# Kernel tuning notes

Measured on AMD Instinct MI355X. Metric: run time of the kernel, lower is better.

## Reference

```python
import jax, jax.numpy as jnp
import numpy as np

N_ATOM_FEATS = 64
N_RBF = 10
N_CONV = 3
N_HIDDEN = 64
N_NODES = 50000
N_EDGES = 800000
N_GRAPHS = 512


def setup_inputs() -> dict:
    key = jax.random.key(0)
    ks = jax.random.split(key, 32)
    d = {}
    d["x_ids"] = jax.random.randint(ks[0], (N_NODES,), 0, 95)
    d["edge_index"] = jax.random.randint(ks[1], (2, N_EDGES), 0, N_NODES)
    d["edge_attr"] = jax.random.uniform(ks[2], (N_EDGES,), jnp.float32) * 6.0  # distances in [0,6)
    d["batch"] = jnp.sort(jax.random.randint(ks[3], (N_NODES,), 0, N_GRAPHS))
    # parameters
    def lin(k, fan_in, shape):
        return jax.random.normal(k, shape, jnp.float32) / np.sqrt(fan_in)
    d["emb"] = jax.random.normal(ks[4], (95, N_ATOM_FEATS), jnp.float32)
    d["blk_W1"] = lin(ks[5], N_ATOM_FEATS, (N_CONV, N_ATOM_FEATS, N_ATOM_FEATS))
    d["blk_b1"] = jnp.zeros((N_CONV, N_ATOM_FEATS), jnp.float32)
    d["blk_We"] = lin(ks[6], N_RBF, (N_CONV, N_RBF, N_ATOM_FEATS))
    d["blk_be"] = jnp.zeros((N_CONV, N_ATOM_FEATS), jnp.float32)
    d["blk_W2"] = lin(ks[7], N_ATOM_FEATS, (N_CONV, N_ATOM_FEATS, N_ATOM_FEATS))
    d["blk_b2"] = jnp.zeros((N_CONV, N_ATOM_FEATS), jnp.float32)
    d["Ws"] = lin(ks[8], N_ATOM_FEATS, (N_ATOM_FEATS, 2 * N_HIDDEN))
    d["bs"] = jnp.zeros((2 * N_HIDDEN,), jnp.float32)
    d["Wbg1"] = lin(ks[9], 2 * N_HIDDEN, (2 * N_HIDDEN, N_HIDDEN))
    d["bbg1"] = jnp.zeros((N_HIDDEN,), jnp.float32)
    d["Wbg2"] = lin(ks[10], N_HIDDEN, (N_HIDDEN, 1))
    d["bbg2"] = jnp.zeros((1,), jnp.float32)
    d["Weh1"] = lin(ks[11], 2 * N_HIDDEN, (2 * N_HIDDEN, N_HIDDEN))
    d["beh1"] = jnp.zeros((N_HIDDEN,), jnp.float32)
    d["Weh2"] = lin(ks[12], N_HIDDEN, (N_HIDDEN, 1))
    d["beh2"] = jnp.zeros((1,), jnp.float32)
    return d


def reference(x_ids, edge_index, edge_attr, batch, emb,
              blk_W1, blk_b1, blk_We, blk_be, blk_W2, blk_b2,
              Ws, bs, Wbg1, bbg1, Wbg2, bbg2, Weh1, beh1, Weh2, beh2):
    src, dst = edge_index[0], edge_index[1]
    # embedding lookup [N, F]
    x = emb[x_ids]
    # Gaussian smearing RBF: [E, n_rbf]
    offset = jnp.linspace(0.0, 6.0, N_RBF).astype(edge_attr.dtype)
    coeff = -0.5 / (offset[1] - offset[0]) ** 2
    e = jnp.exp(coeff * (edge_attr[:, None] - offset) ** 2)
    # interaction blocks (SchNet-style CFConv with residual)
    for i in range(N_CONV):
        h = x @ blk_W1[i] + blk_b1[i]                     # [N, F]
        f = e @ blk_We[i] + blk_be[i]                     # [E, F] edge filters
        m = h[src] * f                                    # [E, F] messages
        agg = jax.ops.segment_sum(m, dst, num_segments=N_NODES)
        x = x + agg @ blk_W2[i] + blk_b2[i]
        x = jax.nn.softplus(x)
    # global mean pool over graphs
    sums = jax.ops.segment_sum(x, batch, num_segments=N_GRAPHS)
    cnts = jax.ops.segment_sum(jnp.ones((x.shape[0],), x.dtype), batch, num_segments=N_GRAPHS)
    c = sums / jnp.maximum(cnts, 1.0)[:, None]
    c = jax.nn.relu(c @ Ws + bs)                          # [G, 2H]
    out_bg = jax.nn.relu(c @ Wbg1 + bbg1) @ Wbg2 + bbg2   # [G, 1]
    out_eh = jax.nn.relu(c @ Weh1 + beh1) @ Weh2 + beh2   # [G, 1]
    return (out_bg, out_eh)
```

## Files before the change

### kernel.cpp

```cpp
#include <hip/hip_runtime.h>
#include <hip/hip_fp16.h>
#include <cstddef>


#define RBF_C0 1.0f
#define RBF_C1 0.60653065971f
#define RBF_C2 0.13533528324f
#define RBF_C3 0.011108996538f
#define RBF_C4 3.3546262790e-4f
#define RBF_C5 3.7266531720e-6f
#define RBF_C6 1.5229979745e-8f
#define RBF_C7 2.2897348457e-11f
#define RBF_C8 1.2664165549e-14f
#define RBF_C9 2.5767043600e-18f

__device__ __forceinline__ float softplusf(float v) {
    return fmaxf(v, 0.0f) + log1pf(__expf(-fabsf(v)));
}

__device__ __forceinline__ float row_gemv(const float4* __restrict__ xr,
                                          const float w[64], float bj) {
    float a0 = bj, a1 = 0.f, a2 = 0.f, a3 = 0.f;
#pragma unroll
    for (int q = 0; q < 4; ++q) {
        float4 v0 = xr[4 * q + 0], v1 = xr[4 * q + 1];
        float4 v2 = xr[4 * q + 2], v3 = xr[4 * q + 3];
        a0 = fmaf(v0.x, w[16 * q + 0], a0);  a0 = fmaf(v0.y, w[16 * q + 1], a0);
        a0 = fmaf(v0.z, w[16 * q + 2], a0);  a0 = fmaf(v0.w, w[16 * q + 3], a0);
        a1 = fmaf(v1.x, w[16 * q + 4], a1);  a1 = fmaf(v1.y, w[16 * q + 5], a1);
        a1 = fmaf(v1.z, w[16 * q + 6], a1);  a1 = fmaf(v1.w, w[16 * q + 7], a1);
        a2 = fmaf(v2.x, w[16 * q + 8], a2);  a2 = fmaf(v2.y, w[16 * q + 9], a2);
        a2 = fmaf(v2.z, w[16 * q + 10], a2); a2 = fmaf(v2.w, w[16 * q + 11], a2);
        a3 = fmaf(v3.x, w[16 * q + 12], a3); a3 = fmaf(v3.y, w[16 * q + 13], a3);
        a3 = fmaf(v3.z, w[16 * q + 14], a3); a3 = fmaf(v3.w, w[16 * q + 15], a3);
    }
    return (a0 + a1) + (a2 + a3);
}

__device__ __forceinline__ float filt_ab(const float wp[10], float bj, float A, float B) {
    float P = wp[9];
    P = fmaf(B, P, wp[8]); P = fmaf(B, P, wp[7]); P = fmaf(B, P, wp[6]);
    P = fmaf(B, P, wp[5]); P = fmaf(B, P, wp[4]); P = fmaf(B, P, wp[3]);
    P = fmaf(B, P, wp[2]); P = fmaf(B, P, wp[1]); P = fmaf(B, P, wp[0]);
    return fmaf(A, P, bj);
}

__global__ void k_pre(const int* __restrict__ dst, int* __restrict__ deg,
                      const int* __restrict__ batch, int* __restrict__ gstart,
                      const int* __restrict__ ids, const float* __restrict__ emb,
                      const float* __restrict__ W1, const float* __restrict__ b1,
                      float* __restrict__ x, __half* __restrict__ hA,
                      int n_edges, int n_nodes, int n_graphs) {
    int tid = blockIdx.x * blockDim.x + threadIdx.x;
    int nth = gridDim.x * blockDim.x;
    for (int e = tid; e < n_edges; e += nth) atomicAdd(&deg[dst[e]], 1);
    for (int n = tid; n < n_nodes; n += nth) {
        int b = batch[n];
        int prev = (n == 0) ? -1 : batch[n - 1];
        for (int g = prev + 1; g <= b; ++g) gstart[g] = n;
        if (n == n_nodes - 1)
            for (int g = b + 1; g <= n_graphs; ++g) gstart[g] = n_nodes;
    }
    int lane = threadIdx.x & 63;
    int gw = __builtin_amdgcn_readfirstlane(tid >> 6);
    int nw = nth >> 6;
    float w[64];
#pragma unroll
    for (int k = 0; k < 64; ++k) w[k] = W1[k * 64 + lane];
    float bj = b1[lane];
    for (int n = gw; n < n_nodes; n += nw) {
        int id = __builtin_amdgcn_readfirstlane(ids[n]);
        const float4* xr = (const float4*)(emb + id * 64);
        float v = row_gemv(xr, w, bj);
        x[n * 64 + lane] = emb[id * 64 + lane];
        hA[n * 64 + lane] = __float2half(v);
    }
}

__global__ void k_scana(const int* __restrict__ deg, int* __restrict__ off_,
                        int* __restrict__ bsum, int n) {
    __shared__ int s[256];
    int i = blockIdx.x * 256 + threadIdx.x;
    int v = (i < n) ? deg[i] : 0;
    s[threadIdx.x] = v;
    __syncthreads();
    for (int off = 1; off < 256; off <<= 1) {
        int t = (threadIdx.x >= off) ? s[threadIdx.x - off] : 0;
        __syncthreads();
        s[threadIdx.x] += t;
        __syncthreads();
    }
    if (i < n) off_[i + 1] = s[threadIdx.x];
    if (threadIdx.x == 255) bsum[blockIdx.x] = s[255];
}

__global__ void k_scanb(int* __restrict__ bsum, int nb) {
    __shared__ int s[256];
    int v = ((int)threadIdx.x < nb) ? bsum[threadIdx.x] : 0;
    s[threadIdx.x] = v;
    __syncthreads();
    for (int off = 1; off < 256; off <<= 1) {
        int t = (threadIdx.x >= off) ? s[threadIdx.x - off] : 0;
        __syncthreads();
        s[threadIdx.x] += t;
        __syncthreads();
    }
    if ((int)threadIdx.x < nb) bsum[threadIdx.x] = s[threadIdx.x] - v;
}

__global__ void k_scanc(const int* __restrict__ deg, const int* __restrict__ bsum,
                        int* __restrict__ off_, int* __restrict__ cursor, int n) {
    int i = blockIdx.x * blockDim.x + threadIdx.x;
    if (i < n) {
        int incl = off_[i + 1] + bsum[i >> 8];
        off_[i + 1] = incl;
        cursor[i] = incl - deg[i];
    }
    if (i == 0) off_[0] = 0;
}

__global__ void k_scatter(const int* __restrict__ src, const int* __restrict__ dst,
                          const float* __restrict__ dist, int* __restrict__ cursor,
                          int4* __restrict__ psort, int n_edges) {
    int e = blockIdx.x * blockDim.x + threadIdx.x;
    if (e >= n_edges) return;
    int t = dst[e];
    int pos = atomicAdd(&cursor[t], 1);
    float d = dist[e];
    float A = __expf(-1.125f * d * d);
    float B = __expf(1.5f * d);
    psort[pos] = make_int4(src[e] << 6, __float_as_int(A), __float_as_int(B), 0);
}

__global__ __launch_bounds__(256, 8) void k_gather(
        const int4* __restrict__ ps, const int* __restrict__ off,
        const __half* __restrict__ h,
        const float* __restrict__ We, const float* __restrict__ be,
        float* __restrict__ agg, int n_nodes) {
    int lane = threadIdx.x & 63;
    int gw = __builtin_amdgcn_readfirstlane((blockIdx.x * blockDim.x + threadIdx.x) >> 6);
    int nw = (gridDim.x * blockDim.x) >> 6;

    const float C[10] = {RBF_C0, RBF_C1, RBF_C2, RBF_C3, RBF_C4,
                         RBF_C5, RBF_C6, RBF_C7, RBF_C8, RBF_C9};
    float wp[10];
#pragma unroll
    for (int r = 0; r < 10; ++r) wp[r] = We[r * 64 + lane] * C[r];
    float bj = be[lane];

    for (int n = gw; n < n_nodes; n += nw) {
        int k0 = off[n], k1 = off[n + 1];
        float acc = 0.0f;
        int k = k0;
        for (; k + 8 <= k1; k += 8) {
            int4 p0 = ps[k + 0], p1 = ps[k + 1], p2 = ps[k + 2], p3 = ps[k + 3];
            int4 p4 = ps[k + 4], p5 = ps[k + 5], p6 = ps[k + 6], p7 = ps[k + 7];
            float g0 = __half2float(h[p0.x + lane]);
            float g1 = __half2float(h[p1.x + lane]);
            float g2 = __half2float(h[p2.x + lane]);
            float g3 = __half2float(h[p3.x + lane]);
            float g4 = __half2float(h[p4.x + lane]);
            float g5 = __half2float(h[p5.x + lane]);
            float g6 = __half2float(h[p6.x + lane]);
            float g7 = __half2float(h[p7.x + lane]);
            acc = fmaf(g0, filt_ab(wp, bj, __int_as_float(p0.y), __int_as_float(p0.z)), acc);
            acc = fmaf(g1, filt_ab(wp, bj, __int_as_float(p1.y), __int_as_float(p1.z)), acc);
            acc = fmaf(g2, filt_ab(wp, bj, __int_as_float(p2.y), __int_as_float(p2.z)), acc);
            acc = fmaf(g3, filt_ab(wp, bj, __int_as_float(p3.y), __int_as_float(p3.z)), acc);
            acc = fmaf(g4, filt_ab(wp, bj, __int_as_float(p4.y), __int_as_float(p4.z)), acc);
            acc = fmaf(g5, filt_ab(wp, bj, __int_as_float(p5.y), __int_as_float(p5.z)), acc);
            acc = fmaf(g6, filt_ab(wp, bj, __int_as_float(p6.y), __int_as_float(p6.z)), acc);
            acc = fmaf(g7, filt_ab(wp, bj, __int_as_float(p7.y), __int_as_float(p7.z)), acc);
        }
        for (; k + 4 <= k1; k += 4) {
            int4 p0 = ps[k + 0], p1 = ps[k + 1], p2 = ps[k + 2], p3 = ps[k + 3];
            float g0 = __half2float(h[p0.x + lane]);
            float g1 = __half2float(h[p1.x + lane]);
            float g2 = __half2float(h[p2.x + lane]);
            float g3 = __half2float(h[p3.x + lane]);
            acc = fmaf(g0, filt_ab(wp, bj, __int_as_float(p0.y), __int_as_float(p0.z)), acc);
            acc = fmaf(g1, filt_ab(wp, bj, __int_as_float(p1.y), __int_as_float(p1.z)), acc);
            acc = fmaf(g2, filt_ab(wp, bj, __int_as_float(p2.y), __int_as_float(p2.z)), acc);
            acc = fmaf(g3, filt_ab(wp, bj, __int_as_float(p3.y), __int_as_float(p3.z)), acc);
        }
        for (; k < k1; ++k) {
            int4 p = ps[k];
            float g = __half2float(h[p.x + lane]);
            acc = fmaf(g, filt_ab(wp, bj, __int_as_float(p.y), __int_as_float(p.z)), acc);
        }
        agg[n * 64 + lane] = acc;
    }
}

__global__ __launch_bounds__(256) void k_epi(
        const float* __restrict__ agg, float* __restrict__ x,
        const float* __restrict__ W2, const float* __restrict__ b2,
        const float* __restrict__ W1n, const float* __restrict__ b1n,
        __half* __restrict__ hout, int n_nodes, int do_next) {
    __shared__ float B1[64 * 65];
    const int t = threadIdx.x;
    const int lane = t & 63;
    const int wid = __builtin_amdgcn_readfirstlane(t >> 6);
    const int base = blockIdx.x << 6;
    const int nv = min(64, n_nodes - base);

#pragma unroll
    for (int i = 0; i < 4; ++i) {
        int f = ((wid * 4 + i) << 8) + (lane << 2);
        int r = f >> 6, c = f & 63;
        int rs = min(r, nv - 1);
        const float4 v = *(const float4*)(agg + (((size_t)(base + rs)) << 6) + c);
        B1[r * 65 + c + 0] = v.x; B1[r * 65 + c + 1] = v.y;
        B1[r * 65 + c + 2] = v.z; B1[r * 65 + c + 3] = v.w;
    }
    __syncthreads();

    float o[16];
#pragma unroll
    for (int jj = 0; jj < 16; ++jj) o[jj] = 0.0f;
#pragma unroll 4
    for (int k = 0; k < 64; ++k) {
        float a = B1[lane * 65 + k];
        const float* w = W2 + (k << 6) + (wid << 4);
#pragma unroll
        for (int jj = 0; jj < 16; ++jj) o[jj] = fmaf(a, w[jj], o[jj]);
    }
    __syncthreads();

#pragma unroll
    for (int i = 0; i < 4; ++i) {
        int f = ((wid * 4 + i) << 8) + (lane << 2);
        int r = f >> 6, c = f & 63;
        int rs = min(r, nv - 1);
        const float4 v = *(const float4*)(x + (((size_t)(base + rs)) << 6) + c);
        B1[r * 65 + c + 0] = v.x; B1[r * 65 + c + 1] = v.y;
        B1[r * 65 + c + 2] = v.z; B1[r * 65 + c + 3] = v.w;
    }
    __syncthreads();

#pragma unroll
    for (int jj = 0; jj < 16; ++jj) {
        int j = (wid << 4) + jj;
        float xv = B1[lane * 65 + j];
        float xn = softplusf(xv + o[jj] + b2[j]);
        B1[lane * 65 + j] = xn;
    }
    __syncthreads();

#pragma unroll
    for (int rr = 0; rr < 16; ++rr) {
        int r = (wid << 4) + rr;
        if (r < nv) x[(((size_t)(base + r)) << 6) + lane] = B1[r * 65 + lane];
    }

    if (do_next) {
        float o2[16];
#pragma unroll
        for (int jj = 0; jj < 16; ++jj) o2[jj] = b1n[(wid << 4) + jj];
#pragma unroll 4
        for (int k = 0; k < 64; ++k) {
            float xk = B1[lane * 65 + k];
            const float* w = W1n + (k << 6) + (wid << 4);
#pragma unroll
            for (int jj = 0; jj < 16; ++jj) o2[jj] = fmaf(xk, w[jj], o2[jj]);
        }
        __syncthreads();
#pragma unroll
        for (int jj = 0; jj < 16; ++jj)
            B1[lane * 65 + (wid << 4) + jj] = o2[jj];
        __syncthreads();
#pragma unroll
        for (int rr = 0; rr < 16; ++rr) {
            int r = (wid << 4) + rr;
            if (r < nv)
                hout[(((size_t)(base + r)) << 6) + lane] = __float2half(B1[r * 65 + lane]);
        }
    }
}

__global__ __launch_bounds__(256, 6) void k_conv(
        const int4* __restrict__ ps, const int* __restrict__ off,
        const __half* __restrict__ h,
        const float* __restrict__ We, const float* __restrict__ be,
        const float* __restrict__ W2, const float* __restrict__ b2,
        const float* __restrict__ W1n, const float* __restrict__ b1n,
        float* __restrict__ x, __half* __restrict__ hout,
        int n_nodes, int do_next) {
    int lane = threadIdx.x & 63;
    int gw = __builtin_amdgcn_readfirstlane((blockIdx.x * blockDim.x + threadIdx.x) >> 6);
    int nw = (gridDim.x * blockDim.x) >> 6;

    const float C[10] = {RBF_C0, RBF_C1, RBF_C2, RBF_C3, RBF_C4,
                         RBF_C5, RBF_C6, RBF_C7, RBF_C8, RBF_C9};
    float wp[10];
#pragma unroll
    for (int r = 0; r < 10; ++r) wp[r] = We[r * 64 + lane] * C[r];
    float bj  = be[lane];
    float b2j = b2[lane];
    float b1j = do_next ? b1n[lane] : 0.0f;

    for (int n = gw; n < n_nodes; n += nw) {
        int k0 = off[n], k1 = off[n + 1];
        float acc = 0.0f;
        int k = k0;
        for (; k + 8 <= k1; k += 8) {
            int4 p0 = ps[k + 0], p1 = ps[k + 1], p2 = ps[k + 2], p3 = ps[k + 3];
            int4 p4 = ps[k + 4], p5 = ps[k + 5], p6 = ps[k + 6], p7 = ps[k + 7];
            float g0 = __half2float(h[p0.x + lane]);
            float g1 = __half2float(h[p1.x + lane]);
            float g2 = __half2float(h[p2.x + lane]);
            float g3 = __half2float(h[p3.x + lane]);
            float g4 = __half2float(h[p4.x + lane]);
            float g5 = __half2float(h[p5.x + lane]);
            float g6 = __half2float(h[p6.x + lane]);
            float g7 = __half2float(h[p7.x + lane]);
            acc = fmaf(g0, filt_ab(wp, bj, __int_as_float(p0.y), __int_as_float(p0.z)), acc);
            acc = fmaf(g1, filt_ab(wp, bj, __int_as_float(p1.y), __int_as_float(p1.z)), acc);
            acc = fmaf(g2, filt_ab(wp, bj, __int_as_float(p2.y), __int_as_float(p2.z)), acc);
            acc = fmaf(g3, filt_ab(wp, bj, __int_as_float(p3.y), __int_as_float(p3.z)), acc);
            acc = fmaf(g4, filt_ab(wp, bj, __int_as_float(p4.y), __int_as_float(p4.z)), acc);
            acc = fmaf(g5, filt_ab(wp, bj, __int_as_float(p5.y), __int_as_float(p5.z)), acc);
            acc = fmaf(g6, filt_ab(wp, bj, __int_as_float(p6.y), __int_as_float(p6.z)), acc);
            acc = fmaf(g7, filt_ab(wp, bj, __int_as_float(p7.y), __int_as_float(p7.z)), acc);
        }
        for (; k + 4 <= k1; k += 4) {
            int4 p0 = ps[k + 0], p1 = ps[k + 1], p2 = ps[k + 2], p3 = ps[k + 3];
            float g0 = __half2float(h[p0.x + lane]);
            float g1 = __half2float(h[p1.x + lane]);
            float g2 = __half2float(h[p2.x + lane]);
            float g3 = __half2float(h[p3.x + lane]);
            acc = fmaf(g0, filt_ab(wp, bj, __int_as_float(p0.y), __int_as_float(p0.z)), acc);
            acc = fmaf(g1, filt_ab(wp, bj, __int_as_float(p1.y), __int_as_float(p1.z)), acc);
            acc = fmaf(g2, filt_ab(wp, bj, __int_as_float(p2.y), __int_as_float(p2.z)), acc);
            acc = fmaf(g3, filt_ab(wp, bj, __int_as_float(p3.y), __int_as_float(p3.z)), acc);
        }
        for (; k < k1; ++k) {
            int4 p = ps[k];
            float g = __half2float(h[p.x + lane]);
            acc = fmaf(g, filt_ab(wp, bj, __int_as_float(p.y), __int_as_float(p.z)), acc);
        }
        float o0 = b2j + x[n * 64 + lane];
        float o1 = 0.f, o2 = 0.f, o3 = 0.f;
#pragma unroll 4
        for (int kk = 0; kk < 16; ++kk) {
            o0 = fmaf(__shfl(acc, kk),      W2[(kk)      * 64 + lane], o0);
            o1 = fmaf(__shfl(acc, kk + 16), W2[(kk + 16) * 64 + lane], o1);
            o2 = fmaf(__shfl(acc, kk + 32), W2[(kk + 32) * 64 + lane], o2);
            o3 = fmaf(__shfl(acc, kk + 48), W2[(kk + 48) * 64 + lane], o3);
        }
        float xn = softplusf((o0 + o1) + (o2 + o3));
        x[n * 64 + lane] = xn;
        if (do_next) {
            float q0 = b1j, q1 = 0.f, q2 = 0.f, q3 = 0.f;
#pragma unroll 4
            for (int kk = 0; kk < 16; ++kk) {
                q0 = fmaf(__shfl(xn, kk),      W1n[(kk)      * 64 + lane], q0);
                q1 = fmaf(__shfl(xn, kk + 16), W1n[(kk + 16) * 64 + lane], q1);
                q2 = fmaf(__shfl(xn, kk + 32), W1n[(kk + 32) * 64 + lane], q2);
                q3 = fmaf(__shfl(xn, kk + 48), W1n[(kk + 48) * 64 + lane], q3);
            }
            hout[n * 64 + lane] = __float2half((q0 + q1) + (q2 + q3));
        }
    }
}

__global__ void k_poolhead(const float* __restrict__ x, const int* __restrict__ gstart,
                           const float* __restrict__ Ws, const float* __restrict__ bs,
                           const float* __restrict__ Wbg1, const float* __restrict__ bbg1,
                           const float* __restrict__ Wbg2, const float* __restrict__ bbg2,
                           const float* __restrict__ Weh1, const float* __restrict__ beh1,
                           const float* __restrict__ Weh2, const float* __restrict__ beh2,
                           float* __restrict__ out, int n_graphs) {
    __shared__ float red[256];
    __shared__ float c[64];
    __shared__ float h1[128];
    int g = blockIdx.x;
    int t = threadIdx.x, j = t & 63, part = t >> 6;
    int s0 = gstart[g], s1 = gstart[g + 1];
    float acc = 0.0f;
    for (int n = s0 + part; n < s1; n += 4) acc += x[n * 64 + j];
    red[t] = acc;
    __syncthreads();
    if (part == 0)
        c[j] = (red[j] + red[64 + j] + red[128 + j] + red[192 + j]) /
               fmaxf((float)(s1 - s0), 1.0f);
    __syncthreads();
    if (t < 128) {
        float av = bs[t];
#pragma unroll 8
        for (int k = 0; k < 64; ++k) av = fmaf(c[k], Ws[k * 128 + t], av);
        h1[t] = fmaxf(av, 0.0f);
    }
    __syncthreads();
    if (t < 128) {
        const float* W1p = (t < 64) ? Wbg1 : Weh1;
        const float* b1p = (t < 64) ? bbg1 : beh1;
        const float* W2p = (t < 64) ? Wbg2 : Weh2;
        float b2v = (t < 64) ? bbg2[0] : beh2[0];
        int ln = t & 63;
        float a2 = b1p[ln];
#pragma unroll 8
        for (int k = 0; k < 128; ++k) a2 = fmaf(h1[k], W1p[k * 64 + ln], a2);
        a2 = fmaxf(a2, 0.0f);
        float pr = a2 * W2p[ln];
#pragma unroll
        for (int off = 32; off > 0; off >>= 1) pr += __shfl_down(pr, off);
        if (ln == 0) out[(t < 64 ? 0 : n_graphs) + g] = pr + b2v;
    }
}

extern "C" void kernel_launch(void* const* d_in, const int* in_sizes, int n_in,
                              void* d_out, int out_size, void* d_ws, size_t ws_size,
                              hipStream_t stream) {
    const int*   x_ids = (const int*)d_in[0];
    const int*   eidx  = (const int*)d_in[1];
    const float* eattr = (const float*)d_in[2];
    const int*   batch = (const int*)d_in[3];
    const float* emb   = (const float*)d_in[4];
    const float* W1    = (const float*)d_in[5];
    const float* b1    = (const float*)d_in[6];
    const float* We    = (const float*)d_in[7];
    const float* be    = (const float*)d_in[8];
    const float* W2    = (const float*)d_in[9];
    const float* b2    = (const float*)d_in[10];
    const float* Ws_   = (const float*)d_in[11];
    const float* bs_   = (const float*)d_in[12];
    const float* Wbg1  = (const float*)d_in[13];
    const float* bbg1  = (const float*)d_in[14];
    const float* Wbg2  = (const float*)d_in[15];
    const float* bbg2  = (const float*)d_in[16];
    const float* Weh1  = (const float*)d_in[17];
    const float* beh1  = (const float*)d_in[18];
    const float* Weh2  = (const float*)d_in[19];
    const float* beh2  = (const float*)d_in[20];

    int n_nodes  = in_sizes[0];
    int n_edges  = in_sizes[2];
    int n_graphs = out_size / 2;
    const int* src = eidx;
    const int* dst = eidx + n_edges;

    size_t base_bytes =
        (size_t)n_nodes * 64 * sizeof(float)
      + (size_t)n_nodes * 64 * sizeof(__half) * 2
      + (size_t)n_edges * sizeof(int4)
      + (size_t)n_nodes * sizeof(int) * 2
      + (size_t)(n_nodes + 1) * sizeof(int)
      + 256 * sizeof(int)
      + (size_t)(n_graphs + 1) * sizeof(int);
    size_t agg_bytes = (size_t)n_nodes * 64 * sizeof(float);
    int use_split = (ws_size >= base_bytes + agg_bytes + 1024) ? 1 : 0;

    char* p = (char*)d_ws;
    float* x     = (float*)p;   p += (size_t)n_nodes * 64 * sizeof(float);
    __half* hA   = (__half*)p;  p += (size_t)n_nodes * 64 * sizeof(__half);
    __half* hB   = (__half*)p;  p += (size_t)n_nodes * 64 * sizeof(__half);
    int4* psort  = (int4*)p;    p += (size_t)n_edges * sizeof(int4);
    int* deg     = (int*)p;     p += (size_t)n_nodes * sizeof(int);
    int* off_    = (int*)p;     p += (size_t)(n_nodes + 1) * sizeof(int);
    int* cursor  = (int*)p;     p += (size_t)n_nodes * sizeof(int);
    int* bsum    = (int*)p;     p += 256 * sizeof(int);
    int* gstart  = (int*)p;     p += (size_t)(n_graphs + 1) * sizeof(int);
    float* agg   = (float*)p;   p += agg_bytes;
    float* out   = (float*)d_out;

    int nchunks = (n_nodes + 255) / 256;
    int nbE = (n_edges + 255) / 256;
    int nbN = (n_nodes + 255) / 256;
    int ntile = (n_nodes + 63) / 64;

    hipMemsetAsync(deg, 0, (size_t)n_nodes * sizeof(int), stream);
    k_pre<<<nbE, 256, 0, stream>>>(dst, deg, batch, gstart, x_ids, emb, W1, b1,
                                   x, hA, n_edges, n_nodes, n_graphs);
    k_scana<<<nchunks, 256, 0, stream>>>(deg, off_, bsum, n_nodes);
    k_scanb<<<1, 256, 0, stream>>>(bsum, nchunks);
    k_scanc<<<nbN, 256, 0, stream>>>(deg, bsum, off_, cursor, n_nodes);
    k_scatter<<<nbE, 256, 0, stream>>>(src, dst, eattr, cursor, psort, n_edges);

    if (use_split) {
        k_gather<<<4096, 256, 0, stream>>>(psort, off_, hA, We, be, agg, n_nodes);
        k_epi<<<ntile, 256, 0, stream>>>(agg, x, W2, b2,
                                         W1 + 4096, b1 + 64, hB, n_nodes, 1);
        k_gather<<<4096, 256, 0, stream>>>(psort, off_, hB, We + 640, be + 64, agg, n_nodes);
        k_epi<<<ntile, 256, 0, stream>>>(agg, x, W2 + 4096, b2 + 64,
                                         W1 + 8192, b1 + 128, hA, n_nodes, 1);
        k_gather<<<4096, 256, 0, stream>>>(psort, off_, hA, We + 1280, be + 128, agg, n_nodes);
        k_epi<<<ntile, 256, 0, stream>>>(agg, x, W2 + 8192, b2 + 128,
                                         nullptr, nullptr, nullptr, n_nodes, 0);
    } else {
        k_conv<<<4096, 256, 0, stream>>>(psort, off_, hA, We, be, W2, b2,
                                         W1 + 4096, b1 + 64, x, hB, n_nodes, 1);
        k_conv<<<4096, 256, 0, stream>>>(psort, off_, hB, We + 640, be + 64,
                                         W2 + 4096, b2 + 64,
                                         W1 + 8192, b1 + 128, x, hA, n_nodes, 1);
        k_conv<<<4096, 256, 0, stream>>>(psort, off_, hA, We + 1280, be + 128,
                                         W2 + 8192, b2 + 128,
                                         nullptr, nullptr, x, nullptr, n_nodes, 0);
    }

    k_poolhead<<<n_graphs, 256, 0, stream>>>(x, gstart, Ws_, bs_, Wbg1, bbg1, Wbg2, bbg2,
                                             Weh1, beh1, Weh2, beh2, out, n_graphs);
}
```

Measured before the change: 385.1 us.

## Split CSR edge scatter into two-pass bucketed scatter for write locality

Replaces the single random-position edge scatter with a two-pass scheme. The first pass scatters edges into coarse buckets of 32 destination nodes. The second pass reads those bucketed edges and scatters them to their final CSR positions, so writes land in a much narrower address range and cache locality improves. This adds an extra read and write of an 800k-entry int4 buffer plus a second kernel launch. The temporary buffer reuses the agg workspace region.

```diff
diff --git a/kernel.cpp b/kernel.cpp
--- a/kernel.cpp
+++ b/kernel.cpp
@@ -2,6 +2,8 @@
 #include <hip/hip_fp16.h>
 #include <cstddef>
 
+
+#define BSHIFT 5
 
 #define RBF_C0 1.0f
 #define RBF_C1 0.60653065971f
@@ -109,14 +111,40 @@
 }
 
 __global__ void k_scanc(const int* __restrict__ deg, const int* __restrict__ bsum,
-                        int* __restrict__ off_, int* __restrict__ cursor, int n) {
+                        int* __restrict__ off_, int* __restrict__ cursor,
+                        int* __restrict__ bcursor, int n) {
     int i = blockIdx.x * blockDim.x + threadIdx.x;
     if (i < n) {
         int incl = off_[i + 1] + bsum[i >> 8];
         off_[i + 1] = incl;
         cursor[i] = incl - deg[i];
-    }
-    if (i == 0) off_[0] = 0;
+        if (((i + 1) & ((1 << BSHIFT) - 1)) == 0)
+            bcursor[(i + 1) >> BSHIFT] = incl;
+    }
+    if (i == 0) { off_[0] = 0; bcursor[0] = 0; }
+}
+
+__global__ void k_scat1(const int* __restrict__ src, const int* __restrict__ dst,
+                        const float* __restrict__ dist, int* __restrict__ bcursor,
+                        int4* __restrict__ tmp, int n_edges) {
+    int e = blockIdx.x * blockDim.x + threadIdx.x;
+    if (e >= n_edges) return;
+    int t = dst[e];
+    int pos = atomicAdd(&bcursor[t >> BSHIFT], 1);
+    float d = dist[e];
+    float A = __expf(-1.125f * d * d);
+    float B = __expf(1.5f * d);
+    tmp[pos] = make_int4(src[e] << 6, __float_as_int(A), __float_as_int(B), t);
+}
+
+__global__ void k_scat2(const int4* __restrict__ tmp, int* __restrict__ cursor,
+                        int4* __restrict__ psort, int n_edges) {
+    int e = blockIdx.x * blockDim.x + threadIdx.x;
+    if (e >= n_edges) return;
+    int4 p = tmp[e];
+    int t = p.w;
+    int pos = atomicAdd(&cursor[t], 1);
+    psort[pos] = p;
 }
 
 __global__ void k_scatter(const int* __restrict__ src, const int* __restrict__ dst,
@@ -439,6 +467,7 @@
     int n_graphs = out_size / 2;
     const int* src = eidx;
     const int* dst = eidx + n_edges;
+    int nbuck = ((n_nodes + (1 << BSHIFT) - 1) >> BSHIFT);
 
     size_t base_bytes =
         (size_t)n_nodes * 64 * sizeof(float)
@@ -447,9 +476,12 @@
       + (size_t)n_nodes * sizeof(int) * 2
       + (size_t)(n_nodes + 1) * sizeof(int)
       + 256 * sizeof(int)
-      + (size_t)(n_graphs + 1) * sizeof(int);
+      + (size_t)(n_graphs + 1) * sizeof(int)
+      + (size_t)(nbuck + 1) * sizeof(int);
     size_t agg_bytes = (size_t)n_nodes * 64 * sizeof(float);
-    int use_split = (ws_size >= base_bytes + agg_bytes + 1024) ? 1 : 0;
+    size_t tmp_bytes = (size_t)n_edges * sizeof(int4);
+    size_t aggtmp_bytes = agg_bytes > tmp_bytes ? agg_bytes : tmp_bytes;
+    int use_split = (ws_size >= base_bytes + aggtmp_bytes + 1024) ? 1 : 0;
 
     char* p = (char*)d_ws;
     float* x     = (float*)p;   p += (size_t)n_nodes * 64 * sizeof(float);
@@ -461,7 +493,9 @@
     int* cursor  = (int*)p;     p += (size_t)n_nodes * sizeof(int);
     int* bsum    = (int*)p;     p += 256 * sizeof(int);
     int* gstart  = (int*)p;     p += (size_t)(n_graphs + 1) * sizeof(int);
-    float* agg   = (float*)p;   p += agg_bytes;
+    int* bcursor = (int*)p;     p += (size_t)(nbuck + 1) * sizeof(int);
+    float* agg   = (float*)p;
+    int4* tmp    = (int4*)p;
     float* out   = (float*)d_out;
 
     int nchunks = (n_nodes + 255) / 256;
@@ -474,10 +508,11 @@
                                    x, hA, n_edges, n_nodes, n_graphs);
     k_scana<<<nchunks, 256, 0, stream>>>(deg, off_, bsum, n_nodes);
     k_scanb<<<1, 256, 0, stream>>>(bsum, nchunks);
-    k_scanc<<<nbN, 256, 0, stream>>>(deg, bsum, off_, cursor, n_nodes);
-    k_scatter<<<nbE, 256, 0, stream>>>(src, dst, eattr, cursor, psort, n_edges);
+    k_scanc<<<nbN, 256, 0, stream>>>(deg, bsum, off_, cursor, bcursor, n_nodes);
 
     if (use_split) {
+        k_scat1<<<nbE, 256, 0, stream>>>(src, dst, eattr, bcursor, tmp, n_edges);
+        k_scat2<<<nbE, 256, 0, stream>>>(tmp, cursor, psort, n_edges);
         k_gather<<<4096, 256, 0, stream>>>(psort, off_, hA, We, be, agg, n_nodes);
         k_epi<<<ntile, 256, 0, stream>>>(agg, x, W2, b2,
                                          W1 + 4096, b1 + 64, hB, n_nodes, 1);
@@ -488,6 +523,7 @@
         k_epi<<<ntile, 256, 0, stream>>>(agg, x, W2 + 8192, b2 + 128,
                                          nullptr, nullptr, nullptr, n_nodes, 0);
     } else {
+        k_scatter<<<nbE, 256, 0, stream>>>(src, dst, eattr, cursor, psort, n_edges);
         k_conv<<<4096, 256, 0, stream>>>(psort, off_, hA, We, be, W2, b2,
                                          W1 + 4096, b1 + 64, x, hB, n_nodes, 1);
         k_conv<<<4096, 256, 0, stream>>>(psort, off_, hB, We + 640, be + 64,
```

New measurement: 491.4 us. 1.28x slower.

## Replace random atomic edge scatter with two-pass bucketed counting sort

Applied to the files above, without the earlier changes.

Edge sorting by destination now runs in two passes instead of one. First, each block bins 1024 edges into 256-node buckets in shared memory and writes them contiguously into a temporary buffer at per-bucket cursors. Second, one block per bucket places edges into their final CSR slots. The aim is to replace scattered 16-byte global writes and contended global atomics with locality-friendly writes. In exchange it adds an extra full pass over the edge payload, reuses the aggregation buffer as scratch, and only handles up to 256 buckets in the shared histogram.

```diff
diff --git a/kernel.cpp b/kernel.cpp
--- a/kernel.cpp
+++ b/kernel.cpp
@@ -2,6 +2,8 @@
 #include <hip/hip_fp16.h>
 #include <cstddef>
 
+
+#define BSH 8
 
 #define RBF_C0 1.0f
 #define RBF_C1 0.60653065971f
@@ -109,14 +111,96 @@
 }
 
 __global__ void k_scanc(const int* __restrict__ deg, const int* __restrict__ bsum,
-                        int* __restrict__ off_, int* __restrict__ cursor, int n) {
+                        int* __restrict__ off_, int* __restrict__ cursor,
+                        int* __restrict__ bcursor, int n) {
     int i = blockIdx.x * blockDim.x + threadIdx.x;
     if (i < n) {
         int incl = off_[i + 1] + bsum[i >> 8];
         off_[i + 1] = incl;
         cursor[i] = incl - deg[i];
-    }
-    if (i == 0) off_[0] = 0;
+        if (((i + 1) & ((1 << BSH) - 1)) == 0)
+            bcursor[(i + 1) >> BSH] = incl;
+    }
+    if (i == 0) { off_[0] = 0; bcursor[0] = 0; }
+}
+
+__global__ __launch_bounds__(256) void k_scat1(
+        const int* __restrict__ src, const int* __restrict__ dst,
+        const float* __restrict__ dist, int* __restrict__ bcursor,
+        int4* __restrict__ tmp, int n_edges) {
+    __shared__ int hist[256], sofs[256], hbase[256], lcur[256];
+    __shared__ int4 buf[1024];
+    const int t = threadIdx.x;
+    const int base = blockIdx.x << 10;
+
+    hist[t] = 0;
+    __syncthreads();
+
+    int bk[4]; int4 pl[4];
+#pragma unroll
+    for (int i = 0; i < 4; ++i) {
+        int e = base + (i << 8) + t;
+        if (e < n_edges) {
+            int d_ = dst[e];
+            float dd = dist[e];
+            float A = __expf(-1.125f * dd * dd);
+            float B = __expf(1.5f * dd);
+            pl[i] = make_int4(src[e] << 6, __float_as_int(A), __float_as_int(B), d_);
+            bk[i] = d_ >> BSH;
+            atomicAdd(&hist[bk[i]], 1);
+        } else bk[i] = -1;
+    }
+    __syncthreads();
+
+    int mycnt = hist[t];
+    for (int off = 1; off < 256; off <<= 1) {
+        int v = (t >= off) ? hist[t - off] : 0;
+        __syncthreads();
+        hist[t] += v;
+        __syncthreads();
+    }
+    sofs[t] = hist[t] - mycnt;
+    lcur[t] = hist[t] - mycnt;
+    if (mycnt > 0) hbase[t] = atomicAdd(&bcursor[t], mycnt);
+    __syncthreads();
+
+#pragma unroll
+    for (int i = 0; i < 4; ++i) {
+        if (bk[i] >= 0) {
+            int ls = atomicAdd(&lcur[bk[i]], 1);
+            buf[ls] = pl[i];
+        }
+    }
+    __syncthreads();
+
+    int tot = n_edges - base; if (tot > 1024) tot = 1024;
+    for (int s = t; s < tot; s += 256) {
+        int4 p = buf[s];
+        int b = p.w >> BSH;
+        tmp[hbase[b] + (s - sofs[b])] = p;
+    }
+}
+
+__global__ __launch_bounds__(256) void k_scat2(
+        const int4* __restrict__ tmp, const int* __restrict__ off_,
+        int* __restrict__ cursor, int4* __restrict__ psort, int n_nodes) {
+    int b = blockIdx.x;
+    int s0 = off_[b << BSH];
+    int hi = (b + 1) << BSH; if (hi > n_nodes) hi = n_nodes;
+    int s1 = off_[hi];
+    int s = s0 + threadIdx.x;
+    for (; s + 768 < s1; s += 1024) {
+        int4 p0 = tmp[s], p1 = tmp[s + 256], p2 = tmp[s + 512], p3 = tmp[s + 768];
+        int q0 = atomicAdd(&cursor[p0.w], 1);
+        int q1 = atomicAdd(&cursor[p1.w], 1);
+        int q2 = atomicAdd(&cursor[p2.w], 1);
+        int q3 = atomicAdd(&cursor[p3.w], 1);
+        psort[q0] = p0; psort[q1] = p1; psort[q2] = p2; psort[q3] = p3;
+    }
+    for (; s < s1; s += 256) {
+        int4 p = tmp[s];
+        psort[atomicAdd(&cursor[p.w], 1)] = p;
+    }
 }
 
 __global__ void k_scatter(const int* __restrict__ src, const int* __restrict__ dst,
@@ -439,6 +523,8 @@
     int n_graphs = out_size / 2;
     const int* src = eidx;
     const int* dst = eidx + n_edges;
+    int nbuck = (n_nodes + (1 << BSH) - 1) >> BSH;
+    int nbc = (nbuck < 256 ? 256 : nbuck) + 4;
 
     size_t base_bytes =
         (size_t)n_nodes * 64 * sizeof(float)
@@ -447,9 +533,12 @@
       + (size_t)n_nodes * sizeof(int) * 2
       + (size_t)(n_nodes + 1) * sizeof(int)
       + 256 * sizeof(int)
-      + (size_t)(n_graphs + 1) * sizeof(int);
+      + (size_t)(n_graphs + 1) * sizeof(int)
+      + (size_t)nbc * sizeof(int);
     size_t agg_bytes = (size_t)n_nodes * 64 * sizeof(float);
-    int use_split = (ws_size >= base_bytes + agg_bytes + 1024) ? 1 : 0;
+    size_t tmp_bytes = (size_t)n_edges * sizeof(int4);
+    size_t aggtmp_bytes = agg_bytes > tmp_bytes ? agg_bytes : tmp_bytes;
+    int use_split = (ws_size >= base_bytes + aggtmp_bytes + 1024) ? 1 : 0;
 
     char* p = (char*)d_ws;
     float* x     = (float*)p;   p += (size_t)n_nodes * 64 * sizeof(float);
@@ -461,23 +550,27 @@
     int* cursor  = (int*)p;     p += (size_t)n_nodes * sizeof(int);
     int* bsum    = (int*)p;     p += 256 * sizeof(int);
     int* gstart  = (int*)p;     p += (size_t)(n_graphs + 1) * sizeof(int);
-    float* agg   = (float*)p;   p += agg_bytes;
+    int* bcursor = (int*)p;     p += (size_t)nbc * sizeof(int);
+    float* agg   = (float*)p;
+    int4* tmp    = (int4*)p;
     float* out   = (float*)d_out;
 
     int nchunks = (n_nodes + 255) / 256;
     int nbE = (n_edges + 255) / 256;
     int nbN = (n_nodes + 255) / 256;
     int ntile = (n_nodes + 63) / 64;
+    int nbS1 = (n_edges + 1023) / 1024;
 
     hipMemsetAsync(deg, 0, (size_t)n_nodes * sizeof(int), stream);
     k_pre<<<nbE, 256, 0, stream>>>(dst, deg, batch, gstart, x_ids, emb, W1, b1,
                                    x, hA, n_edges, n_nodes, n_graphs);
     k_scana<<<nchunks, 256, 0, stream>>>(deg, off_, bsum, n_nodes);
     k_scanb<<<1, 256, 0, stream>>>(bsum, nchunks);
-    k_scanc<<<nbN, 256, 0, stream>>>(deg, bsum, off_, cursor, n_nodes);
-    k_scatter<<<nbE, 256, 0, stream>>>(src, dst, eattr, cursor, psort, n_edges);
+    k_scanc<<<nbN, 256, 0, stream>>>(deg, bsum, off_, cursor, bcursor, n_nodes);
 
     if (use_split) {
+        k_scat1<<<nbS1, 256, 0, stream>>>(src, dst, eattr, bcursor, tmp, n_edges);
+        k_scat2<<<nbuck, 256, 0, stream>>>(tmp, off_, cursor, psort, n_nodes);
         k_gather<<<4096, 256, 0, stream>>>(psort, off_, hA, We, be, agg, n_nodes);
         k_epi<<<ntile, 256, 0, stream>>>(agg, x, W2, b2,
                                          W1 + 4096, b1 + 64, hB, n_nodes, 1);
@@ -488,6 +581,7 @@
         k_epi<<<ntile, 256, 0, stream>>>(agg, x, W2 + 8192, b2 + 128,
                                          nullptr, nullptr, nullptr, n_nodes, 0);
     } else {
+        k_scatter<<<nbE, 256, 0, stream>>>(src, dst, eattr, cursor, psort, n_edges);
         k_conv<<<4096, 256, 0, stream>>>(psort, off_, hA, We, be, W2, b2,
                                          W1 + 4096, b1 + 64, x, hB, n_nodes, 1);
         k_conv<<<4096, 256, 0, stream>>>(psort, off_, hB, We + 640, be + 64,
```

New measurement: 384.6 us. No clear change (-0.1%).
